# Kernel tuning notes

Hardware: AMD Instinct MI355X
Metric: run time of the kernel (lower is better)

The kernel has to match this reference:

```python
import jax, jax.numpy as jnp
import numpy as np

N_EMBD = 768
N_HEAD = 12
N_LAYERS = 12
VOCAB = 50257
HEAD_DIM = N_EMBD // N_HEAD
D_FF = 4 * N_EMBD
B, S = 2, 1024


def setup_inputs() -> dict:
    key = jax.random.key(0)
    ks = jax.random.split(key, 8)
    w = lambda k, shape: jax.random.normal(k, shape, jnp.float32) * 0.02
    return {
        "x": jax.random.normal(ks[0], (B, S, N_EMBD), jnp.float32),
        "Wqkv": w(ks[1], (N_LAYERS, N_EMBD, 3 * N_EMBD)),
        "bqkv": jnp.zeros((N_LAYERS, 3 * N_EMBD), jnp.float32),
        "Wo": w(ks[2], (N_LAYERS, N_EMBD, N_EMBD)),
        "bo": jnp.zeros((N_LAYERS, N_EMBD), jnp.float32),
        "W1": w(ks[3], (N_LAYERS, N_EMBD, D_FF)),
        "b1": jnp.zeros((N_LAYERS, D_FF), jnp.float32),
        "W2": w(ks[4], (N_LAYERS, D_FF, N_EMBD)),
        "b2": jnp.zeros((N_LAYERS, N_EMBD), jnp.float32),
        "ln1_g": jnp.ones((N_LAYERS, N_EMBD), jnp.float32),
        "ln1_b": jnp.zeros((N_LAYERS, N_EMBD), jnp.float32),
        "ln2_g": jnp.ones((N_LAYERS, N_EMBD), jnp.float32),
        "ln2_b": jnp.zeros((N_LAYERS, N_EMBD), jnp.float32),
        "lnf_g": jnp.ones((N_EMBD,), jnp.float32),
        "lnf_b": jnp.zeros((N_EMBD,), jnp.float32),
        "Wlm": w(ks[5], (VOCAB, N_EMBD)),
    }


def layer_norm(x, g, b, eps=1e-5):
    m = jnp.mean(x, axis=-1, keepdims=True)
    v = jnp.var(x, axis=-1, keepdims=True)
    return (x - m) * jax.lax.rsqrt(v + eps) * g + b


def reference(x, Wqkv, bqkv, Wo, bo, W1, b1, W2, b2,
              ln1_g, ln1_b, ln2_g, ln2_b, lnf_g, lnf_b, Wlm):
    b_, s_, d_ = x.shape
    # additive causal mask: (1 - tril) * -1e10
    mask = (1.0 - jnp.tril(jnp.ones((s_, s_), jnp.float32))) * -1e10
    scale = 1.0 / np.sqrt(HEAD_DIM).astype(np.float32)

    def block(h, p):
        wqkv, bq, wo, bo_, w1, b1_, w2, b2_, g1, be1, g2, be2 = p
        a = layer_norm(h, g1, be1)
        qkv = a @ wqkv + bq                      # [B,S,3D]
        q, k, v = jnp.split(qkv, 3, axis=-1)
        split = lambda t: t.reshape(b_, s_, N_HEAD, HEAD_DIM).transpose(0, 2, 1, 3)
        q, k, v = split(q), split(k), split(v)   # [B,H,S,hd]
        scores = jnp.einsum('bhqd,bhkd->bhqk', q, k) * scale + mask
        probs = jax.nn.softmax(scores, axis=-1)
        o = jnp.einsum('bhqk,bhkd->bhqd', probs, v)
        o = o.transpose(0, 2, 1, 3).reshape(b_, s_, d_)
        h = h + (o @ wo + bo_)                   # residual 1
        m = layer_norm(h, g2, be2)
        m = jax.nn.gelu(m @ w1 + b1_, approximate=False)  # torch nn.GELU (erf)
        h = h + (m @ w2 + b2_)                   # residual 2
        return h, None

    h, _ = jax.lax.scan(
        block, x,
        (Wqkv, bqkv, Wo, bo, W1, b1, W2, b2, ln1_g, ln1_b, ln2_g, ln2_b))
    h = layer_norm(h, lnf_g, lnf_b)
    return h @ Wlm.T                             # [B,S,VOCAB]
```

## Files before the change

kernel.cpp:

```cpp
#include <hip/hip_runtime.h>
#include <math.h>

typedef unsigned short u16;
typedef u16 u16x8 __attribute__((ext_vector_type(8)));
typedef u16 u16x4 __attribute__((ext_vector_type(4)));
typedef short short8 __attribute__((ext_vector_type(8)));
typedef float f32x4 __attribute__((ext_vector_type(4)));

#define NE 768
#define NH 12
#define NL 12
#define NV 50257
#define NVP 50432
#define HD 64
#define DFF 3072
#define NB 2
#define SL 1024
#define TT 2048
#define QKVD 2304

static __device__ __forceinline__ u16 f2bf(float f){
  unsigned int x; __builtin_memcpy(&x, &f, 4);
  x = (x + 0x7FFFu + ((x >> 16) & 1u)) >> 16;
  return (u16)x;
}

typedef const __attribute__((address_space(1))) unsigned int* gas1_t;
typedef __attribute__((address_space(3))) unsigned int* las3_t;
static __device__ __forceinline__ void gload16(const u16* g, u16* l){
  __builtin_amdgcn_global_load_lds((gas1_t)(const void*)g, (las3_t)(void*)l, 16, 0, 0);
}
static __device__ __forceinline__ void waitvm(int n){
  switch (n){
    case 0: asm volatile("s_waitcnt vmcnt(0)" ::: "memory"); break;
    case 3: asm volatile("s_waitcnt vmcnt(3)" ::: "memory"); break;
    case 4: asm volatile("s_waitcnt vmcnt(4)" ::: "memory"); break;
    case 6: asm volatile("s_waitcnt vmcnt(6)" ::: "memory"); break;
    default: asm volatile("s_waitcnt vmcnt(8)" ::: "memory"); break;
  }
}

__global__ void k_cvt4(const float4* __restrict__ in, u16x4* __restrict__ out, long n4){
  long i = (long)blockIdx.x * blockDim.x + threadIdx.x;
  long st = (long)gridDim.x * blockDim.x;
  for (; i < n4; i += st){
    float4 v = in[i];
    u16x4 o = { f2bf(v.x), f2bf(v.y), f2bf(v.z), f2bf(v.w) };
    out[i] = o;
  }
}

__global__ __launch_bounds__(256) void k_transpose_cvt_all(const float* __restrict__ in0,
    u16* __restrict__ out0, int K, int N){
  __shared__ u16 tile[32][33];
  const float* in = in0 + (long)blockIdx.z * K * N;
  u16* out = out0 + (long)blockIdx.z * N * K;
  int n0 = blockIdx.x * 32, k0 = blockIdx.y * 32;
#pragma unroll
  for (int i = 0; i < 4; ++i){
    int e = threadIdx.x + i * 256;
    int r = e >> 5, c = e & 31;
    tile[r][c] = f2bf(in[(long)(k0 + r) * N + (n0 + c)]);
  }
  __syncthreads();
#pragma unroll
  for (int i = 0; i < 4; ++i){
    int e = threadIdx.x + i * 256;
    int r = e >> 5, c = e & 31;
    out[(long)(n0 + r) * K + (k0 + c)] = tile[c][r];
  }
}

__global__ __launch_bounds__(256) void k_layernorm(const float* __restrict__ x,
    const float* __restrict__ g, const float* __restrict__ b, u16* __restrict__ out){
  int row = blockIdx.x;
  const float* xr = x + (long)row * NE;
  int t = threadIdx.x;
  float v[3];
  v[0] = xr[t]; v[1] = xr[t + 256]; v[2] = xr[t + 512];
  float s = v[0] + v[1] + v[2];
  float sq = v[0]*v[0] + v[1]*v[1] + v[2]*v[2];
  __shared__ float red[8];
#pragma unroll
  for (int o = 32; o; o >>= 1){ s += __shfl_xor(s, o); sq += __shfl_xor(sq, o); }
  int wid = t >> 6, lane = t & 63;
  if (!lane){ red[wid] = s; red[4 + wid] = sq; }
  __syncthreads();
  s  = red[0] + red[1] + red[2] + red[3];
  sq = red[4] + red[5] + red[6] + red[7];
  float mean = s * (1.f / NE);
  float var  = sq * (1.f / NE) - mean * mean;
  float rs = rsqrtf(var + 1e-5f);
  u16* orow = out + (long)row * NE;
#pragma unroll
  for (int i = 0; i < 3; ++i){
    int c = t + i * 256;
    orow[c] = f2bf((v[i] - mean) * rs * g[c] + b[c]);
  }
}

__global__ __launch_bounds__(256) void k_combine_ln(float* __restrict__ h,
    const float* __restrict__ part, const float* __restrict__ bias, int nsplit,
    const float* __restrict__ g, const float* __restrict__ b, u16* __restrict__ aout){
  int row = blockIdx.x;
  int t = threadIdx.x;
  float* hr = h + (long)row * NE;
  float v[3];
#pragma unroll
  for (int i = 0; i < 3; ++i){
    int c = t + i * 256;
    float acc = hr[c] + bias[c];
    for (int s = 0; s < nsplit; ++s)
      acc += part[(long)s * TT * NE + (long)row * NE + c];
    v[i] = acc;
    hr[c] = acc;
  }
  float s = v[0] + v[1] + v[2];
  float sq = v[0]*v[0] + v[1]*v[1] + v[2]*v[2];
  __shared__ float red[8];
#pragma unroll
  for (int o = 32; o; o >>= 1){ s += __shfl_xor(s, o); sq += __shfl_xor(sq, o); }
  int wid = t >> 6, lane = t & 63;
  if (!lane){ red[wid] = s; red[4 + wid] = sq; }
  __syncthreads();
  s  = red[0] + red[1] + red[2] + red[3];
  sq = red[4] + red[5] + red[6] + red[7];
  float mean = s * (1.f / NE);
  float var  = sq * (1.f / NE) - mean * mean;
  float rs = rsqrtf(var + 1e-5f);
  u16* orow = aout + (long)row * NE;
#pragma unroll
  for (int i = 0; i < 3; ++i){
    int c = t + i * 256;
    orow[c] = f2bf((v[i] - mean) * rs * g[c] + b[c]);
  }
}

__global__ __launch_bounds__(128) void k_flash(const u16* __restrict__ qkv,
    const u16* __restrict__ vt, u16* __restrict__ out){
  __shared__ u16 Ps[2][16][72];
  const int z = blockIdx.x;
  const int qt = gridDim.y - 1 - blockIdx.y;
  const int b = z / NH, h = z % NH;
  const int t = threadIdx.x, lane = t & 63, wid = t >> 6;
  const int lr = lane & 15, lk = lane >> 4;
  const int qr0 = qt * 32 + wid * 16;
  const u16* Qp = qkv + (long)(b * SL + qr0 + lr) * QKVD + h * HD;
  short8 aq[2];
  aq[0] = *(const short8*)(Qp + lk * 8);
  aq[1] = *(const short8*)(Qp + 32 + lk * 8);
  const u16* Kb  = qkv + (long)(b * SL) * QKVD + NE + h * HD;
  const u16* Vtb = vt + (long)z * HD * SL;
  f32x4 o[4] = {};
  float m[4], l[4];
#pragma unroll
  for (int r = 0; r < 4; ++r){ m[r] = -3e38f; l[r] = 0.f; }
  const int nt = (qt * 32 + 31) / 64 + 1;
  for (int kt = 0; kt < nt; ++kt){
    const int kv0 = kt * 64;
    short8 kb[4][2];
#pragma unroll
    for (int j = 0; j < 4; ++j)
#pragma unroll
      for (int c = 0; c < 2; ++c)
        kb[j][c] = *(const short8*)(Kb + (long)(kv0 + j * 16 + lr) * QKVD + c * 32 + lk * 8);
    f32x4 s[4] = {};
#pragma unroll
    for (int c = 0; c < 2; ++c)
#pragma unroll
      for (int j = 0; j < 4; ++j)
        s[j] = __builtin_amdgcn_mfma_f32_16x16x32_bf16(aq[c], kb[j][c], s[j], 0, 0, 0);
    const bool dm = (kt == nt - 1);
#pragma unroll
    for (int r = 0; r < 4; ++r){
      const int row = qr0 + lk * 4 + r;
      float pm = -3e38f;
#pragma unroll
      for (int j = 0; j < 4; ++j){
        float v = s[j][r] * 0.125f;
        if (dm && (kv0 + j * 16 + lr > row)) v = -3e38f;
        s[j][r] = v;
        pm = fmaxf(pm, v);
      }
#pragma unroll
      for (int off = 1; off < 16; off <<= 1) pm = fmaxf(pm, __shfl_xor(pm, off));
      float mn = fmaxf(m[r], pm);
      float f = __expf(m[r] - mn);
      m[r] = mn;
      float ps = 0.f;
#pragma unroll
      for (int j = 0; j < 4; ++j){
        float pv = __expf(s[j][r] - mn);
        ps += pv;
        Ps[wid][lk * 4 + r][j * 16 + lr] = f2bf(pv);
      }
#pragma unroll
      for (int off = 1; off < 16; off <<= 1) ps += __shfl_xor(ps, off);
      l[r] = l[r] * f + ps;
#pragma unroll
      for (int j = 0; j < 4; ++j) o[j][r] *= f;
    }
#pragma unroll
    for (int c = 0; c < 2; ++c){
      short8 pa = *(const short8*)&Ps[wid][lr][c * 32 + lk * 8];
#pragma unroll
      for (int j = 0; j < 4; ++j){
        short8 vb = *(const short8*)(Vtb + (long)(j * 16 + lr) * SL + kv0 + c * 32 + lk * 8);
        o[j] = __builtin_amdgcn_mfma_f32_16x16x32_bf16(pa, vb, o[j], 0, 0, 0);
      }
    }
  }
  u16* O = out + (long)(b * SL) * NE + h * HD;
#pragma unroll
  for (int r = 0; r < 4; ++r){
    float inv = 1.f / l[r];
    const int row = qr0 + lk * 4 + r;
#pragma unroll
    for (int j = 0; j < 4; ++j)
      O[(long)row * NE + j * 16 + lr] = f2bf(o[j][r] * inv);
  }
}

struct GemmP {
  const u16* A; const u16* B; void* C;
  const float* bias; u16* vt;
  int M, N, K, lda, ldb, ldc, mode;
  long zA, zB, zC;
};

__global__ __launch_bounds__(256) void k_gemm_bt(GemmP p){
  __shared__ u16 As[3][64 * 32];
  __shared__ u16 Bs[3][128 * 32];
  const int nwg = gridDim.x * gridDim.y;
  const int orig = blockIdx.x + blockIdx.y * gridDim.x;
  const int wg = (orig & 7) * (nwg >> 3) + (orig >> 3);
  const int m0 = (wg % gridDim.x) * 64, n0 = (wg / gridDim.x) * 128;
  const u16* A = p.A + (long)blockIdx.z * p.zA;
  const u16* B = p.B + (long)blockIdx.z * p.zB;
  const long offC = (long)blockIdx.z * p.zC;
  const int t = threadIdx.x, lane = t & 63, wid = t >> 6;
  const int wm = (wid >> 1) * 32, wn = (wid & 1) * 64;
  const int lr = lane & 15, lk = lane >> 4;
  const int srow = t >> 2;
  const int sseg = (t & 3) * 8;
  const u16* Abase  = A + (long)(m0 + srow) * p.lda + sseg;
  const u16* Bbase  = B + (long)(n0 + srow) * p.ldb + sseg;
  const u16* Bbase2 = B + (long)(n0 + 64 + srow) * p.ldb + sseg;
  auto stage = [&](int buf, int kt){
    gload16(Abase  + kt * 32, &As[buf][t * 8]);
    gload16(Bbase  + kt * 32, &Bs[buf][t * 8]);
    gload16(Bbase2 + kt * 32, &Bs[buf][(t + 256) * 8]);
  };
  f32x4 acc[2][4] = {};
  const int nk = p.K >> 5;
  stage(0, 0);
  stage(1, 1);
  int cur = 0;
  for (int kt = 0; kt < nk; ++kt){
    if (kt + 2 < nk){
      int nxt = cur + 2; if (nxt >= 3) nxt -= 3;
      stage(nxt, kt + 2);
    }
    int rem = nk - 1 - kt;
    waitvm(rem >= 2 ? 6 : rem == 1 ? 3 : 0);
    __builtin_amdgcn_s_barrier();
    short8 af[2], bfr[4];
#pragma unroll
    for (int i = 0; i < 2; ++i) af[i]  = *(const short8*)&As[cur][(wm + i * 16 + lr) * 32 + lk * 8];
#pragma unroll
    for (int j = 0; j < 4; ++j) bfr[j] = *(const short8*)&Bs[cur][(wn + j * 16 + lr) * 32 + lk * 8];
#pragma unroll
    for (int i = 0; i < 2; ++i)
#pragma unroll
      for (int j = 0; j < 4; ++j)
        acc[i][j] = __builtin_amdgcn_mfma_f32_16x16x32_bf16(af[i], bfr[j], acc[i][j], 0, 0, 0);
    asm volatile("s_waitcnt lgkmcnt(0)" ::: "memory");
    __builtin_amdgcn_s_barrier();
    cur = (cur == 2) ? 0 : cur + 1;
  }
#pragma unroll
  for (int i = 0; i < 2; ++i){
#pragma unroll
    for (int r = 0; r < 4; ++r){
      int row = m0 + wm + i * 16 + lk * 4 + r;
      if (row >= p.M) continue;
#pragma unroll
      for (int j = 0; j < 4; ++j){
        int col = n0 + wn + j * 16 + lr;
        if (col >= p.N) continue;
        float v = acc[i][j][r];
        long idx = offC + (long)row * p.ldc + col;
        if (p.mode == 5){
          v += p.bias[col];
          if (col >= 2 * NE){
            int d = col - 2 * NE;
            long vidx = (((long)(row >> 10) * NH + (d >> 6)) * HD + (d & 63)) * SL + (row & 1023);
            p.vt[vidx] = f2bf(v);
          } else {
            ((u16*)p.C)[idx] = f2bf(v);
          }
        } else if (p.mode == 2){
          v += p.bias[col];
          v = 0.5f * v * (1.f + erff(v * 0.70710678118f));
          ((u16*)p.C)[idx] = f2bf(v);
        } else {
          ((float*)p.C)[idx] = v;
        }
      }
    }
  }
}

static inline void gemm(hipStream_t s, const u16* A, int lda, const u16* B, int ldb,
    void* C, int ldc, int M, int N, int K, const float* bias, u16* vt, int mode,
    int gz = 1, long zA = 0, long zB = 0, long zC = 0){
  GemmP p{ A, B, C, bias, vt, M, N, K, lda, ldb, ldc, mode, zA, zB, zC };
  dim3 g(M / 64, (N + 127) / 128, gz);
  k_gemm_bt<<<g, 256, 0, s>>>(p);
}

__global__ __launch_bounds__(512, 1) void k_gemm256(const u16* __restrict__ A,
    const u16* __restrict__ B, float* __restrict__ C){
  __shared__ u16 As[3][256 * 32];
  __shared__ u16 Bs[3][256 * 32];
  const int gx = gridDim.x, nwg = gx * gridDim.y;
  const int orig = blockIdx.x + blockIdx.y * gx;
  const int wg = (orig & 7) * (nwg >> 3) + (orig >> 3);
  const int m0 = (wg % gx) * 256, n0 = (wg / gx) * 256;
  const int t = threadIdx.x, lane = t & 63;
  const int lr = lane & 15, lk = lane >> 4;
  const int wid = t >> 6, wr = wid >> 2, wc = wid & 3;
  const u16* gA[2]; const u16* gB[2]; int ldst[2];
#pragma unroll
  for (int i = 0; i < 2; ++i){
    int idx = t + i * 512, r = idx >> 2, pp = idx & 3, sl = pp ^ (r & 3);
    gA[i] = A + (long)(m0 + r) * NE + sl * 8;
    gB[i] = B + (long)(n0 + r) * NE + sl * 8;
    ldst[i] = idx * 8;
  }
  auto stage = [&](int buf, int kt){
#pragma unroll
    for (int i = 0; i < 2; ++i) gload16(gA[i] + kt * 32, &As[buf][ldst[i]]);
#pragma unroll
    for (int i = 0; i < 2; ++i) gload16(gB[i] + kt * 32, &Bs[buf][ldst[i]]);
  };
  f32x4 acc[8][4] = {};
  const int nk = NE / 32;
  stage(0, 0);
  stage(1, 1);
  int cur = 0;
  for (int kt = 0; kt < nk; ++kt){
    if (kt + 2 < nk){
      int nxt = cur + 2; if (nxt >= 3) nxt -= 3;
      stage(nxt, kt + 2);
    }
    int rem = nk - 1 - kt;
    waitvm(rem >= 2 ? 8 : rem == 1 ? 4 : 0);
    __builtin_amdgcn_sched_barrier(0);
    __builtin_amdgcn_s_barrier();
    __builtin_amdgcn_sched_barrier(0);
    short8 bf[4];
#pragma unroll
    for (int nj = 0; nj < 4; ++nj){
      int r = wc * 64 + nj * 16 + lr;
      bf[nj] = *(const short8*)&Bs[cur][r * 32 + ((lk ^ (r & 3)) * 8)];
    }
    {
      short8 af[4];
#pragma unroll
      for (int mi = 0; mi < 4; ++mi){
        int r = wr * 128 + mi * 16 + lr;
        af[mi] = *(const short8*)&As[cur][r * 32 + ((lk ^ (r & 3)) * 8)];
      }
      __builtin_amdgcn_s_setprio(1);
#pragma unroll
      for (int mi = 0; mi < 4; ++mi)
#pragma unroll
        for (int nj = 0; nj < 4; ++nj)
          acc[mi][nj] = __builtin_amdgcn_mfma_f32_16x16x32_bf16(af[mi], bf[nj], acc[mi][nj], 0, 0, 0);
      __builtin_amdgcn_s_setprio(0);
    }
    {
      short8 af[4];
#pragma unroll
      for (int mi = 0; mi < 4; ++mi){
        int r = wr * 128 + (mi + 4) * 16 + lr;
        af[mi] = *(const short8*)&As[cur][r * 32 + ((lk ^ (r & 3)) * 8)];
      }
      __builtin_amdgcn_s_setprio(1);
#pragma unroll
      for (int mi = 0; mi < 4; ++mi)
#pragma unroll
        for (int nj = 0; nj < 4; ++nj)
          acc[mi + 4][nj] = __builtin_amdgcn_mfma_f32_16x16x32_bf16(af[mi], bf[nj], acc[mi + 4][nj], 0, 0, 0);
      __builtin_amdgcn_s_setprio(0);
    }
    asm volatile("s_waitcnt lgkmcnt(0)" ::: "memory");
    __builtin_amdgcn_sched_barrier(0);
    __builtin_amdgcn_s_barrier();
    cur = (cur == 2) ? 0 : cur + 1;
  }
#pragma unroll
  for (int mi = 0; mi < 8; ++mi)
#pragma unroll
    for (int r = 0; r < 4; ++r){
      int row = m0 + wr * 128 + mi * 16 + lk * 4 + r;
#pragma unroll
      for (int nj = 0; nj < 4; ++nj){
        int col = n0 + wc * 64 + nj * 16 + lr;
        if (col < NV) C[(long)row * NV + col] = acc[mi][nj][r];
      }
    }
}

extern "C" void kernel_launch(void* const* d_in, const int* in_sizes, int n_in,
                              void* d_out, int out_size, void* d_ws, size_t ws_size,
                              hipStream_t stream){
  (void)in_sizes; (void)n_in; (void)out_size; (void)ws_size;
  const float* x    = (const float*)d_in[0];
  const float* Wqkv = (const float*)d_in[1];
  const float* bqkv = (const float*)d_in[2];
  const float* Wo   = (const float*)d_in[3];
  const float* bo   = (const float*)d_in[4];
  const float* W1   = (const float*)d_in[5];
  const float* b1   = (const float*)d_in[6];
  const float* W2   = (const float*)d_in[7];
  const float* b2   = (const float*)d_in[8];
  const float* ln1g = (const float*)d_in[9];
  const float* ln1b = (const float*)d_in[10];
  const float* ln2g = (const float*)d_in[11];
  const float* ln2b = (const float*)d_in[12];
  const float* lnfg = (const float*)d_in[13];
  const float* lnfb = (const float*)d_in[14];
  const float* Wlm  = (const float*)d_in[15];

  char* ws = (char*)d_ws;
  size_t off = 0;
  auto alloc = [&](size_t bytes){ void* p = ws + off; off += (bytes + 255) & ~255UL; return p; };
  float* h      = (float*)alloc((size_t)TT * NE * 4);
  u16*   a      = (u16*)  alloc((size_t)TT * NE * 2);
  u16*   qkv    = (u16*)  alloc((size_t)TT * QKVD * 2);
  u16*   vtbuf  = (u16*)  alloc((size_t)NB * NH * HD * SL * 2);
  u16*   attno  = (u16*)  alloc((size_t)TT * NE * 2);
  u16*   ffm    = (u16*)  alloc((size_t)TT * DFF * 2);
  float* part   = (float*)alloc((size_t)4 * TT * NE * 4);
  u16*   wqkvT  = (u16*)  alloc((size_t)NL * QKVD * NE * 2);
  u16*   woT    = (u16*)  alloc((size_t)NL * NE * NE * 2);
  u16*   w1T    = (u16*)  alloc((size_t)NL * DFF * NE * 2);
  u16*   w2T    = (u16*)  alloc((size_t)NL * NE * DFF * 2);
  u16*   wlmB   = (u16*)  alloc((size_t)NVP * NE * 2);

  hipMemcpyAsync(h, x, (size_t)TT * NE * 4, hipMemcpyDeviceToDevice, stream);
  k_transpose_cvt_all<<<dim3(QKVD / 32, NE / 32, NL), 256, 0, stream>>>(Wqkv, wqkvT, NE, QKVD);
  k_transpose_cvt_all<<<dim3(NE / 32, NE / 32, NL),   256, 0, stream>>>(Wo,   woT,   NE, NE);
  k_transpose_cvt_all<<<dim3(DFF / 32, NE / 32, NL),  256, 0, stream>>>(W1,   w1T,   NE, DFF);
  k_transpose_cvt_all<<<dim3(NE / 32, DFF / 32, NL),  256, 0, stream>>>(W2,   w2T,   DFF, NE);
  k_cvt4<<<2048, 256, 0, stream>>>((const float4*)Wlm, (u16x4*)wlmB, (long)NV * NE / 4);
  hipMemsetAsync(wlmB + (size_t)NV * NE, 0, (size_t)(NVP - NV) * NE * 2, stream);

  k_layernorm<<<TT, 256, 0, stream>>>(h, ln1g, ln1b, a);

  for (int L = 0; L < NL; ++L){
    gemm(stream, a, NE, wqkvT + (size_t)L * QKVD * NE, NE, qkv, QKVD, TT, QKVD, NE,
         bqkv + (size_t)L * QKVD, vtbuf, 5);
    k_flash<<<dim3(NB * NH, SL / 32), 128, 0, stream>>>(qkv, vtbuf, attno);
    gemm(stream, attno, NE, woT + (size_t)L * NE * NE, NE, part, NE, TT, NE, 384,
         nullptr, nullptr, 3, 2, 384, 384, (long)TT * NE);
    k_combine_ln<<<TT, 256, 0, stream>>>(h, part, bo + (size_t)L * NE, 2,
         ln2g + (size_t)L * NE, ln2b + (size_t)L * NE, a);
    gemm(stream, a, NE, w1T + (size_t)L * DFF * NE, NE, ffm, DFF, TT, DFF, NE,
         b1 + (size_t)L * DFF, nullptr, 2);
    gemm(stream, ffm, DFF, w2T + (size_t)L * NE * DFF, DFF, part, NE, TT, NE, 768,
         nullptr, nullptr, 3, 4, 768, 768, (long)TT * NE);
    const float* gn = (L + 1 < NL) ? ln1g + (size_t)(L + 1) * NE : lnfg;
    const float* bn = (L + 1 < NL) ? ln1b + (size_t)(L + 1) * NE : lnfb;
    k_combine_ln<<<TT, 256, 0, stream>>>(h, part, b2 + (size_t)L * NE, 4, gn, bn, a);
  }
  k_gemm256<<<dim3(TT / 256, NVP / 256), 512, 0, stream>>>(a, wlmB, (float*)d_out);
}
```

Before: 2.474 ms.

## Vectorize weight transpose, XOR-swizzle GEMM LDS tiles, double-buffer LM-head GEMM

The weight transpose/convert kernel now handles 128-column tiles, reading float4 and writing 4-element bf16 vectors, which cuts the number of small memory transactions. Both GEMM kernels change their LDS layout to an XOR swizzle keyed on (row>>1)&3, aimed at reducing bank conflicts when MFMA fragments are read. The LM-head GEMM moves from triple to double buffering and raises its launch-bounds occupancy hint, trading prefetch depth for lower LDS use and possibly more resident workgroups. The higher occupancy hint may also limit registers for the large accumulator array and cause spills.

```diff
diff --git a/kernel.cpp b/kernel.cpp
--- a/kernel.cpp
+++ b/kernel.cpp
@@ -52,22 +52,29 @@
 
 __global__ __launch_bounds__(256) void k_transpose_cvt_all(const float* __restrict__ in0,
     u16* __restrict__ out0, int K, int N){
-  __shared__ u16 tile[32][33];
+  __shared__ u16 tile[128][33];
   const float* in = in0 + (long)blockIdx.z * K * N;
   u16* out = out0 + (long)blockIdx.z * N * K;
-  int n0 = blockIdx.x * 32, k0 = blockIdx.y * 32;
+  const int n0 = blockIdx.x * 128, k0 = blockIdx.y * 32;
+  const int t = threadIdx.x;
 #pragma unroll
   for (int i = 0; i < 4; ++i){
-    int e = threadIdx.x + i * 256;
+    int e = t + i * 256;
     int r = e >> 5, c = e & 31;
-    tile[r][c] = f2bf(in[(long)(k0 + r) * N + (n0 + c)]);
+    float4 v = *(const float4*)(in + (long)(k0 + r) * N + n0 + c * 4);
+    tile[c * 4 + 0][r] = f2bf(v.x);
+    tile[c * 4 + 1][r] = f2bf(v.y);
+    tile[c * 4 + 2][r] = f2bf(v.z);
+    tile[c * 4 + 3][r] = f2bf(v.w);
   }
   __syncthreads();
 #pragma unroll
   for (int i = 0; i < 4; ++i){
-    int e = threadIdx.x + i * 256;
-    int r = e >> 5, c = e & 31;
-    out[(long)(n0 + r) * K + (k0 + c)] = tile[c][r];
+    int e = t + i * 256;
+    int nr = e >> 3, kc = e & 7;
+    u16x4 o = { tile[nr][kc * 4 + 0], tile[nr][kc * 4 + 1],
+                tile[nr][kc * 4 + 2], tile[nr][kc * 4 + 3] };
+    *(u16x4*)(out + (long)(n0 + nr) * K + k0 + kc * 4) = o;
   }
 }
 
@@ -242,7 +249,7 @@
   const int wm = (wid >> 1) * 32, wn = (wid & 1) * 64;
   const int lr = lane & 15, lk = lane >> 4;
   const int srow = t >> 2;
-  const int sseg = (t & 3) * 8;
+  const int sseg = ((t & 3) ^ ((srow >> 1) & 3)) * 8;
   const u16* Abase  = A + (long)(m0 + srow) * p.lda + sseg;
   const u16* Bbase  = B + (long)(n0 + srow) * p.ldb + sseg;
   const u16* Bbase2 = B + (long)(n0 + 64 + srow) * p.ldb + sseg;
@@ -266,9 +273,15 @@
     __builtin_amdgcn_s_barrier();
     short8 af[2], bfr[4];
 #pragma unroll
-    for (int i = 0; i < 2; ++i) af[i]  = *(const short8*)&As[cur][(wm + i * 16 + lr) * 32 + lk * 8];
-#pragma unroll
-    for (int j = 0; j < 4; ++j) bfr[j] = *(const short8*)&Bs[cur][(wn + j * 16 + lr) * 32 + lk * 8];
+    for (int i = 0; i < 2; ++i){
+      int r = wm + i * 16 + lr;
+      af[i]  = *(const short8*)&As[cur][r * 32 + ((lk ^ ((r >> 1) & 3)) * 8)];
+    }
+#pragma unroll
+    for (int j = 0; j < 4; ++j){
+      int r = wn + j * 16 + lr;
+      bfr[j] = *(const short8*)&Bs[cur][r * 32 + ((lk ^ ((r >> 1) & 3)) * 8)];
+    }
 #pragma unroll
     for (int i = 0; i < 2; ++i)
 #pragma unroll
@@ -319,10 +332,10 @@
   k_gemm_bt<<<g, 256, 0, s>>>(p);
 }
 
-__global__ __launch_bounds__(512, 1) void k_gemm256(const u16* __restrict__ A,
+__global__ __launch_bounds__(512, 4) void k_gemm256(const u16* __restrict__ A,
     const u16* __restrict__ B, float* __restrict__ C){
-  __shared__ u16 As[3][256 * 32];
-  __shared__ u16 Bs[3][256 * 32];
+  __shared__ u16 As[2][256 * 32];
+  __shared__ u16 Bs[2][256 * 32];
   const int gx = gridDim.x, nwg = gx * gridDim.y;
   const int orig = blockIdx.x + blockIdx.y * gx;
   const int wg = (orig & 7) * (nwg >> 3) + (orig >> 3);
@@ -333,7 +346,7 @@
   const u16* gA[2]; const u16* gB[2]; int ldst[2];
 #pragma unroll
   for (int i = 0; i < 2; ++i){
-    int idx = t + i * 512, r = idx >> 2, pp = idx & 3, sl = pp ^ (r & 3);
+    int idx = t + i * 512, r = idx >> 2, pp = idx & 3, sl = pp ^ ((r >> 1) & 3);
     gA[i] = A + (long)(m0 + r) * NE + sl * 8;
     gB[i] = B + (long)(n0 + r) * NE + sl * 8;
     ldst[i] = idx * 8;
@@ -347,15 +360,10 @@
   f32x4 acc[8][4] = {};
   const int nk = NE / 32;
   stage(0, 0);
-  stage(1, 1);
-  int cur = 0;
   for (int kt = 0; kt < nk; ++kt){
-    if (kt + 2 < nk){
-      int nxt = cur + 2; if (nxt >= 3) nxt -= 3;
-      stage(nxt, kt + 2);
-    }
-    int rem = nk - 1 - kt;
-    waitvm(rem >= 2 ? 8 : rem == 1 ? 4 : 0);
+    const int buf = kt & 1;
+    if (kt + 1 < nk){ stage(buf ^ 1, kt + 1); waitvm(4); }
+    else            { waitvm(0); }
     __builtin_amdgcn_sched_barrier(0);
     __builtin_amdgcn_s_barrier();
     __builtin_amdgcn_sched_barrier(0);
@@ -363,14 +371,14 @@
 #pragma unroll
     for (int nj = 0; nj < 4; ++nj){
       int r = wc * 64 + nj * 16 + lr;
-      bf[nj] = *(const short8*)&Bs[cur][r * 32 + ((lk ^ (r & 3)) * 8)];
+      bf[nj] = *(const short8*)&Bs[buf][r * 32 + ((lk ^ ((r >> 1) & 3)) * 8)];
     }
     {
       short8 af[4];
 #pragma unroll
       for (int mi = 0; mi < 4; ++mi){
         int r = wr * 128 + mi * 16 + lr;
-        af[mi] = *(const short8*)&As[cur][r * 32 + ((lk ^ (r & 3)) * 8)];
+        af[mi] = *(const short8*)&As[buf][r * 32 + ((lk ^ ((r >> 1) & 3)) * 8)];
       }
       __builtin_amdgcn_s_setprio(1);
 #pragma unroll
@@ -385,7 +393,7 @@
 #pragma unroll
       for (int mi = 0; mi < 4; ++mi){
         int r = wr * 128 + (mi + 4) * 16 + lr;
-        af[mi] = *(const short8*)&As[cur][r * 32 + ((lk ^ (r & 3)) * 8)];
+        af[mi] = *(const short8*)&As[buf][r * 32 + ((lk ^ ((r >> 1) & 3)) * 8)];
       }
       __builtin_amdgcn_s_setprio(1);
 #pragma unroll
@@ -398,7 +406,6 @@
     asm volatile("s_waitcnt lgkmcnt(0)" ::: "memory");
     __builtin_amdgcn_sched_barrier(0);
     __builtin_amdgcn_s_barrier();
-    cur = (cur == 2) ? 0 : cur + 1;
   }
 #pragma unroll
   for (int mi = 0; mi < 8; ++mi)
@@ -451,10 +458,10 @@
   u16*   wlmB   = (u16*)  alloc((size_t)NVP * NE * 2);
 
   hipMemcpyAsync(h, x, (size_t)TT * NE * 4, hipMemcpyDeviceToDevice, stream);
-  k_transpose_cvt_all<<<dim3(QKVD / 32, NE / 32, NL), 256, 0, stream>>>(Wqkv, wqkvT, NE, QKVD);
-  k_transpose_cvt_all<<<dim3(NE / 32, NE / 32, NL),   256, 0, stream>>>(Wo,   woT,   NE, NE);
-  k_transpose_cvt_all<<<dim3(DFF / 32, NE / 32, NL),  256, 0, stream>>>(W1,   w1T,   NE, DFF);
-  k_transpose_cvt_all<<<dim3(NE / 32, DFF / 32, NL),  256, 0, stream>>>(W2,   w2T,   DFF, NE);
+  k_transpose_cvt_all<<<dim3(QKVD / 128, NE / 32, NL), 256, 0, stream>>>(Wqkv, wqkvT, NE, QKVD);
+  k_transpose_cvt_all<<<dim3(NE / 128, NE / 32, NL),   256, 0, stream>>>(Wo,   woT,   NE, NE);
+  k_transpose_cvt_all<<<dim3(DFF / 128, NE / 32, NL),  256, 0, stream>>>(W1,   w1T,   NE, DFF);
+  k_transpose_cvt_all<<<dim3(NE / 128, DFF / 32, NL),  256, 0, stream>>>(W2,   w2T,   DFF, NE);
   k_cvt4<<<2048, 256, 0, stream>>>((const float4*)Wlm, (u16x4*)wlmB, (long)NV * NE / 4);
   hipMemsetAsync(wlmB + (size_t)NV * NE, 0, (size_t)(NVP - NV) * NE * 2, stream);
 
```

Result: slower. 3.468 ms (+40.2%).
